# Kernel tuning notes

Hardware: AMD Instinct MI355X
Metric: run time of the kernel (lower is better)

Reference implementation:

```python
import jax, jax.numpy as jnp
import numpy as np
import math

B, S, H, HKV, DH = 2, 2048, 32, 1, 128  # batch, seq, q heads, kv heads, per-head/model dim
D_K = 128


def setup_inputs() -> dict:
    key = jax.random.key(0)
    ks = jax.random.split(key, 11)
    sc = 0.02
    return {
        "query": jax.random.normal(ks[0], (B, S, DH), jnp.float32),
        "key": jax.random.normal(ks[1], (B, S, DH), jnp.float32),
        "values": jax.random.normal(ks[2], (B, S, DH), jnp.float32),
        "W_q": jax.random.normal(ks[3], (DH, H * DH), jnp.float32) * sc,
        "b_q": jnp.zeros((H * DH,), jnp.float32),
        "W_k": jax.random.normal(ks[4], (DH, HKV * DH), jnp.float32) * sc,
        "b_k": jnp.zeros((HKV * DH,), jnp.float32),
        "W_v": jax.random.normal(ks[5], (DH, HKV * DH), jnp.float32) * sc,
        "b_v": jnp.zeros((HKV * DH,), jnp.float32),
        "W_o": jax.random.normal(ks[6], (H * DH, DH), jnp.float32) * sc,
        "b_o": jnp.zeros((DH,), jnp.float32),
    }


def reference(query, key, values, W_q, b_q, W_k, b_k, W_v, b_v, W_o, b_o):
    # Projections (note: the original uses raw .view(-1, H, S, DH), which we
    # replicate exactly — it is a reshape, not a transpose).
    q = (query @ W_q + b_q).reshape(-1, H, S, DH)      # [B,H,S,DH]
    k = (key @ W_k + b_k).reshape(-1, HKV, S, DH)       # [B,1,S,DH]
    v = (values @ W_v + b_v).reshape(-1, HKV, S, DH)    # [B,1,S,DH]

    # RoPE outputs in the original forward are computed but never used
    # (dead code), and mask defaults to None -> no masking. Dropout omitted
    # for deterministic reference.
    scores = jnp.matmul(q, jnp.swapaxes(k, -1, -2)) / math.sqrt(D_K)  # [B,H,S,S]
    attn = jax.nn.softmax(scores, axis=-1)
    out = jnp.matmul(attn, v)                           # [B,H,S,DH]
    out = jnp.swapaxes(out, 1, 2).reshape(-1, S, H * DH)
    return out @ W_o + b_o                              # [B,S,DH]
```

## Files before the change

kernel.cpp:

```cpp
#include <hip/hip_runtime.h>
#include <hip/hip_bf16.h>
#include <math.h>


typedef __hip_bfloat16 bf16;
typedef __attribute__((ext_vector_type(8))) short short8;
typedef __attribute__((ext_vector_type(4))) float floatx4;

static constexpr int B_ = 2;
static constexpr int S_ = 2048;
static constexpr int H_ = 32;
static constexpr int DH_ = 128;

#define GL16(gp, lp)                                              \
  __builtin_amdgcn_global_load_lds(                               \
      (const __attribute__((address_space(1))) void*)(gp),        \
      (__attribute__((address_space(3))) void*)(lp), 16, 0, 0)

static __device__ __forceinline__ unsigned bpack(float lo, float hi) {
  unsigned a = __float_as_uint(lo) + 0x8000u;
  unsigned b = __float_as_uint(hi) + 0x8000u;
  return __builtin_amdgcn_perm(b, a, 0x07060302u);
}

static __device__ __forceinline__ bool detect_f32(
    const unsigned short* __restrict__ q) {
  int t = threadIdx.x & 63;
  int cnt = 0;
#pragma unroll
  for (int i = 0; i < 8; ++i) {
    unsigned short u = q[t * 8 + i];
    int e = (u >> 7) & 0xFF;
    if (e < 0x60) cnt++;
  }
#pragma unroll
  for (int off = 1; off < 64; off <<= 1) cnt += __shfl_xor(cnt, off);
  return cnt >= 8;
}

static __device__ __forceinline__ short8 loadA8(const void* __restrict__ base,
                                                size_t elt, bool f) {
  if (f) {
    const float4* p = (const float4*)((const float*)base + elt);
    float4 x = p[0], y = p[1];
    union { unsigned u[4]; short8 v; } r;
    r.u[0] = bpack(x.x, x.y);
    r.u[1] = bpack(x.z, x.w);
    r.u[2] = bpack(y.x, y.y);
    r.u[3] = bpack(y.z, y.w);
    return r.v;
  }
  return *(const short8*)((const bf16*)base + elt);
}

static __device__ void do_ttranspose(const void* __restrict__ W,
                                     bf16* __restrict__ Wt, int K, int N,
                                     bool f, float scale, int bx, int by,
                                     bf16 (*tile)[66]) {
  int n0 = bx * 64, k0 = by * 64;
  int c = threadIdx.x & 63;
  int r4 = threadIdx.x >> 6;
#pragma unroll
  for (int i = 0; i < 16; ++i) {
    int r = r4 * 16 + i;
    float v = f ? ((const float*)W)[(size_t)(k0 + r) * N + n0 + c]
                : __bfloat162float(((const bf16*)W)[(size_t)(k0 + r) * N + n0 + c]);
    tile[r][c] = __float2bfloat16(v * scale);
  }
  __syncthreads();
#pragma unroll
  for (int i = 0; i < 16; ++i) {
    int cc = r4 * 16 + i;
    Wt[(size_t)(n0 + cc) * K + k0 + c] = tile[c][cc];
  }
}

__global__ void prep(const void* __restrict__ query,
                     const void* __restrict__ bq, const void* __restrict__ bk,
                     const void* __restrict__ bv, const void* __restrict__ bo,
                     float* __restrict__ fbq, float* __restrict__ fbk,
                     float* __restrict__ fbv, float* __restrict__ fbo,
                     const void* __restrict__ Wq, bf16* __restrict__ Wqt,
                     const void* __restrict__ Wk, bf16* __restrict__ Wkt,
                     const void* __restrict__ Wv, bf16* __restrict__ Wvt,
                     const void* __restrict__ Wo, bf16* __restrict__ Wot,
                     float qscale) {
  __shared__ bf16 tile[64][66];
  const int id = blockIdx.x;
  const bool f = detect_f32((const unsigned short*)query);
  if (id < 18) {
    int i = id * 256 + threadIdx.x;
    const void* s; float* d; int off; float sc = 1.f;
    if (i < 4096) { s = bq; d = fbq; off = i; sc = qscale; }
    else if (i < 4224) { s = bk; d = fbk; off = i - 4096; }
    else if (i < 4352) { s = bv; d = fbv; off = i - 4224; }
    else if (i < 4480) { s = bo; d = fbo; off = i - 4352; }
    else return;
    float v = f ? ((const float*)s)[off]
                : __bfloat162float(((const bf16*)s)[off]);
    d[off] = v * sc;
  } else if (id < 146) {
    int j = id - 18;
    do_ttranspose(Wq, Wqt, DH_, H_ * DH_, f, qscale, j % 64, j / 64, tile);
  } else if (id < 150) {
    int j = id - 146;
    do_ttranspose(Wk, Wkt, DH_, DH_, f, 1.0f, j % 2, j / 2, tile);
  } else if (id < 154) {
    int j = id - 150;
    do_ttranspose(Wv, Wvt, DH_, DH_, f, 1.0f, j % 2, j / 2, tile);
  } else {
    int j = id - 154;
    do_ttranspose(Wo, Wot, H_ * DH_, DH_, f, 1.0f, j % 2, j / 2, tile);
  }
}

__global__ __launch_bounds__(256) void gemm_qkv(
    const void* __restrict__ query, const void* __restrict__ key,
    const void* __restrict__ values, const bf16* __restrict__ Wqt,
    const bf16* __restrict__ Wkt, const bf16* __restrict__ Wvt,
    const float* __restrict__ fbq, const float* __restrict__ fbk,
    const float* __restrict__ fbv, bf16* __restrict__ Qp,
    bf16* __restrict__ Kp, bf16* __restrict__ Vtp) {
  const int bx = blockIdx.x;
  const void* A; const bf16* Bt; const float* bias; bf16* Cb;
  int mode, ldc, colb;
  if (bx < 64)      { A = query;  Bt = Wqt; bias = fbq; Cb = Qp;  mode = 0; ldc = 4096; colb = bx; }
  else if (bx < 66) { A = key;    Bt = Wkt; bias = fbk; Cb = Kp;  mode = 0; ldc = 128;  colb = bx - 64; }
  else              { A = values; Bt = Wvt; bias = fbv; Cb = Vtp; mode = 3; ldc = 0;    colb = bx - 66; }

  const bool f = detect_f32((const unsigned short*)query);
  const int lane = threadIdx.x & 63;
  const int wave = threadIdx.x >> 6;
  const int lm = lane & 15;
  const int quad = lane >> 4;
  const int row_base = blockIdx.y * 64 + wave * 16;
  const int col_base = colb * 64;

  const size_t aelt = (size_t)(row_base + lm) * DH_ + quad * 8;
  const bf16* brow = Bt + (size_t)(col_base + lm) * DH_ + quad * 8;

  floatx4 z = {0.f, 0.f, 0.f, 0.f};
  floatx4 acc[4] = {z, z, z, z};
#pragma unroll
  for (int kk = 0; kk < DH_; kk += 32) {
    short8 a = loadA8(A, aelt + kk, f);
#pragma unroll
    for (int t = 0; t < 4; ++t) {
      short8 b = *(const short8*)(brow + (size_t)(t * 16) * DH_ + kk);
      acc[t] = __builtin_amdgcn_mfma_f32_16x16x32_bf16(a, b, acc[t], 0, 0, 0);
    }
  }
#pragma unroll
  for (int t = 0; t < 4; ++t) {
    int col = col_base + t * 16 + lm;
#pragma unroll
    for (int r = 0; r < 4; ++r) {
      int row = row_base + quad * 4 + r;
      if (mode == 0) {
        Cb[(size_t)row * ldc + col] = __float2bfloat16(acc[t][r] + bias[col]);
      } else {
        Cb[((size_t)((row >> 11) * DH_ + col)) * S_ + (row & 2047)] =
            __float2bfloat16(acc[t][r] + bias[col]);
      }
    }
  }
}

__global__ __launch_bounds__(256) void gemm_out(
    const bf16* __restrict__ A, const bf16* __restrict__ Bt,
    float* __restrict__ Cf) {
  constexpr int K_len = (H_ * DH_) / 8;
  const int lane = threadIdx.x & 63;
  const int wave = threadIdx.x >> 6;
  const int lm = lane & 15;
  const int quad = lane >> 4;
  const int row_base = blockIdx.x * 64 + wave * 16;
  const int koff = blockIdx.y * K_len;

  const bf16* arow = A + (size_t)(row_base + lm) * (H_ * DH_) + koff + quad * 8;
  const bf16* brow = Bt + (size_t)lm * (H_ * DH_) + koff + quad * 8;

  floatx4 z = {0.f, 0.f, 0.f, 0.f};
  floatx4 acc[8] = {z, z, z, z, z, z, z, z};
#pragma unroll 2
  for (int kk = 0; kk < K_len; kk += 32) {
    short8 a = *(const short8*)(arow + kk);
#pragma unroll
    for (int t = 0; t < 8; ++t) {
      short8 b = *(const short8*)(brow + (size_t)(t * 16) * (H_ * DH_) + kk);
      acc[t] = __builtin_amdgcn_mfma_f32_16x16x32_bf16(a, b, acc[t], 0, 0, 0);
    }
  }
#pragma unroll
  for (int t = 0; t < 8; ++t) {
    int col = t * 16 + lm;
#pragma unroll
    for (int r = 0; r < 4; ++r) {
      int row = row_base + quad * 4 + r;
      Cf[(size_t)blockIdx.y * (4096 * 128) + (size_t)row * DH_ + col] =
          acc[t][r];
    }
  }
}

__global__ void finish_out(const float* __restrict__ parts,
                           const float* __restrict__ bias,
                           float* __restrict__ out) {
  int i = blockIdx.x * 256 + threadIdx.x;
  const float4* p = (const float4*)parts;
  float4 bb = ((const float4*)bias)[i & 31];
  float4 o = bb;
#pragma unroll
  for (int j = 0; j < 8; ++j) {
    float4 a = p[i + (size_t)j * 131072];
    o.x += a.x; o.y += a.y; o.z += a.z; o.w += a.w;
  }
  ((float4*)out)[i] = o;
}

static __device__ __forceinline__ float fexp2(float x) {
#if __has_builtin(__builtin_amdgcn_exp2f)
  return __builtin_amdgcn_exp2f(x);
#else
  return exp2f(x);
#endif
}

static __device__ __forceinline__ void pexchange(const unsigned pk[8],
                                                 int quad, short8* pf) {
  const bool q0 = (quad & 1);
  unsigned sA0 = q0 ? pk[0] : pk[2];
  unsigned sA1 = q0 ? pk[1] : pk[3];
  unsigned sA2 = q0 ? pk[4] : pk[6];
  unsigned sA3 = q0 ? pk[5] : pk[7];
  unsigned r0 = (unsigned)__shfl_xor((int)sA0, 16);
  unsigned r1 = (unsigned)__shfl_xor((int)sA1, 16);
  unsigned r2 = (unsigned)__shfl_xor((int)sA2, 16);
  unsigned r3 = (unsigned)__shfl_xor((int)sA3, 16);
  unsigned M0 = q0 ? r0 : pk[0];
  unsigned M1 = q0 ? r1 : pk[1];
  unsigned M2 = q0 ? pk[2] : r0;
  unsigned M3 = q0 ? pk[3] : r1;
  unsigned M4 = q0 ? r2 : pk[4];
  unsigned M5 = q0 ? r3 : pk[5];
  unsigned M6 = q0 ? pk[6] : r2;
  unsigned M7 = q0 ? pk[7] : r3;
  const bool swp = (quad == 1) || (quad == 2);
  union { unsigned u[4]; short8 v; } f0, f1;
  unsigned t0, t1;
  t0 = (unsigned)__shfl_xor((int)M0, 48); f0.u[0] = swp ? t0 : M0;
  t1 = (unsigned)__shfl_xor((int)M1, 48); f0.u[1] = swp ? t1 : M1;
  t0 = (unsigned)__shfl_xor((int)M2, 48); f0.u[2] = swp ? t0 : M2;
  t1 = (unsigned)__shfl_xor((int)M3, 48); f0.u[3] = swp ? t1 : M3;
  t0 = (unsigned)__shfl_xor((int)M4, 48); f1.u[0] = swp ? t0 : M4;
  t1 = (unsigned)__shfl_xor((int)M5, 48); f1.u[1] = swp ? t1 : M5;
  t0 = (unsigned)__shfl_xor((int)M6, 48); f1.u[2] = swp ? t0 : M6;
  t1 = (unsigned)__shfl_xor((int)M7, 48); f1.u[3] = swp ? t1 : M7;
  pf[0] = f0.v;
  pf[1] = f1.v;
}

__global__ __launch_bounds__(256, 2) void flash_attn(
    const bf16* __restrict__ Qp, const bf16* __restrict__ Kp,
    const bf16* __restrict__ Vt, bf16* __restrict__ O2c) {
  const int tid = threadIdx.x;
  const int lane = tid & 63;
  const int wave = tid >> 6;
  const int lm = lane & 15;
  const int quad = lane >> 4;
  const int qt = blockIdx.x;
  const int h = blockIdx.y;
  const int b = blockIdx.z;

  __shared__ __align__(16) bf16 Klds[64 * 128];
  __shared__ __align__(16) bf16 Vlds[2][128 * 64];

  const int base = qt * 128 + wave * 32;
  const bf16* qrow = Qp + ((size_t)b * S_ + h * 64 + (base >> 5)) * 4096;
  short8 qf0[4], qf1[4];
#pragma unroll
  for (int ks = 0; ks < 4; ++ks) {
    qf0[ks] = *(const short8*)(qrow + lm * 128 + quad * 8 + ks * 32);
    qf1[ks] = *(const short8*)(qrow + (16 + lm) * 128 + quad * 8 + ks * 32);
  }

  const bf16* Kb = Kp + (size_t)b * S_ * DH_;
  const bf16* Vb = Vt + (size_t)b * DH_ * S_;
  const int sw = lm & 7;

  const bf16* kgp[4];
  const bf16* vgp[4];
#pragma unroll
  for (int i = 0; i < 4; ++i) {
    const int inst = wave * 4 + i;
    const int krow = inst * 4 + quad;
    kgp[i] = Kb + (size_t)krow * 128 + ((lm ^ (krow & 7)) * 8);
    const int vrow = inst * 8 + (lane >> 3);
    vgp[i] = Vb + (size_t)vrow * S_ + (((lane & 7) ^ (vrow & 7)) * 8);
  }

  floatx4 z = {0.f, 0.f, 0.f, 0.f};
  floatx4 oa0[8], oa1[8];
#pragma unroll
  for (int nt = 0; nt < 8; ++nt) { oa0[nt] = z; oa1[nt] = z; }
  float ls0 = 0.f, ls1 = 0.f;

#pragma unroll
  for (int i = 0; i < 4; ++i) {
    GL16(kgp[i], &Klds[(wave * 4 + i) * 512]);
    GL16(vgp[i], &Vlds[0][(wave * 4 + i) * 512]);
    kgp[i] += 64 * 128;
    vgp[i] += 64;
  }

  int cur = 0;
  for (int kb = 0; kb < S_; kb += 64) {
    __syncthreads();
    const bool more = kb + 64 < S_;
    if (more) {
#pragma unroll
      for (int i = 0; i < 4; ++i) {
        GL16(vgp[i], &Vlds[cur ^ 1][(wave * 4 + i) * 512]);
        vgp[i] += 64;
      }
    }

    floatx4 s0[4] = {z, z, z, z}, s1[4] = {z, z, z, z};
    __builtin_amdgcn_s_setprio(1);
#pragma unroll
    for (int t = 0; t < 4; ++t) {
#pragma unroll
      for (int ks = 0; ks < 4; ++ks) {
        short8 kf = *(const short8*)(&Klds[(t * 16 + lm) * 128 +
                                           (((quad + 4 * ks) ^ sw) * 8)]);
        s0[t] = __builtin_amdgcn_mfma_f32_16x16x32_bf16(kf, qf0[ks], s0[t],
                                                        0, 0, 0);
        s1[t] = __builtin_amdgcn_mfma_f32_16x16x32_bf16(kf, qf1[ks], s1[t],
                                                        0, 0, 0);
      }
    }
    __builtin_amdgcn_s_setprio(0);

    __syncthreads();
    if (more) {
#pragma unroll
      for (int i = 0; i < 4; ++i) {
        GL16(kgp[i], &Klds[(wave * 4 + i) * 512]);
        kgp[i] += 64 * 128;
      }
    }

    unsigned pk0[8], pk1[8];
#pragma unroll
    for (int t = 0; t < 4; ++t) {
      float a0 = fexp2(s0[t][0]), a1 = fexp2(s0[t][1]);
      float a2 = fexp2(s0[t][2]), a3 = fexp2(s0[t][3]);
      ls0 += (a0 + a1) + (a2 + a3);
      pk0[2 * t] = bpack(a0, a1);
      pk0[2 * t + 1] = bpack(a2, a3);
      float c0 = fexp2(s1[t][0]), c1 = fexp2(s1[t][1]);
      float c2 = fexp2(s1[t][2]), c3 = fexp2(s1[t][3]);
      ls1 += (c0 + c1) + (c2 + c3);
      pk1[2 * t] = bpack(c0, c1);
      pk1[2 * t + 1] = bpack(c2, c3);
    }
    short8 pf0[2], pf1[2];
    pexchange(pk0, quad, pf0);
    pexchange(pk1, quad, pf1);

    __builtin_amdgcn_s_setprio(1);
#pragma unroll
    for (int ks2 = 0; ks2 < 2; ++ks2) {
#pragma unroll
      for (int nt = 0; nt < 8; ++nt) {
        short8 vf = *(const short8*)(&Vlds[cur][(nt * 16 + lm) * 64 +
                                              (((quad + 4 * ks2) ^ sw) * 8)]);
        oa0[nt] = __builtin_amdgcn_mfma_f32_16x16x32_bf16(pf0[ks2], vf,
                                                          oa0[nt], 0, 0, 0);
        oa1[nt] = __builtin_amdgcn_mfma_f32_16x16x32_bf16(pf1[ks2], vf,
                                                          oa1[nt], 0, 0, 0);
      }
    }
    __builtin_amdgcn_s_setprio(0);
    cur ^= 1;
  }

  ls0 += __shfl_xor(ls0, 16);
  ls0 += __shfl_xor(ls0, 32);
  ls1 += __shfl_xor(ls1, 16);
  ls1 += __shfl_xor(ls1, 32);
  float inv0[4], inv1[4];
#pragma unroll
  for (int r = 0; r < 4; ++r) {
    inv0[r] = 1.0f / __shfl(ls0, quad * 4 + r);
    inv1[r] = 1.0f / __shfl(ls1, quad * 4 + r);
  }

#pragma unroll
  for (int r = 0; r < 4; ++r) {
    int s2a = base + quad * 4 + r;
    int s2b = s2a + 16;
    size_t ba = ((size_t)b * S_ + s2a) * 4096 + (size_t)h * 128;
    size_t bb = ((size_t)b * S_ + s2b) * 4096 + (size_t)h * 128;
#pragma unroll
    for (int nt = 0; nt < 8; ++nt) {
      O2c[ba + nt * 16 + lm] = __float2bfloat16(oa0[nt][r] * inv0[r]);
      O2c[bb + nt * 16 + lm] = __float2bfloat16(oa1[nt][r] * inv1[r]);
    }
  }
}

extern "C" void kernel_launch(void* const* d_in, const int* in_sizes, int n_in,
                              void* d_out, int out_size, void* d_ws,
                              size_t ws_size, hipStream_t stream) {
  (void)in_sizes;
  (void)n_in;
  (void)out_size;
  (void)ws_size;

  const void* query = d_in[0];
  const void* key = d_in[1];
  const void* values = d_in[2];
  const void* W_q = d_in[3];
  const void* b_q = d_in[4];
  const void* W_k = d_in[5];
  const void* b_k = d_in[6];
  const void* W_v = d_in[7];
  const void* b_v = d_in[8];
  const void* W_o = d_in[9];
  const void* b_o = d_in[10];
  float* out = (float*)d_out;

  const float kScale = 0.1275174388204085f;
  const int M = B_ * S_;
  const int QN = B_ * S_ * DH_;

  char* w = (char*)d_ws;
  auto carve = [&](size_t bytes) -> char* {
    char* p = w;
    w += (bytes + 255) & ~(size_t)255;
    return p;
  };
  float* fbq = (float*)carve((size_t)H_ * DH_ * 4);
  float* fbk = (float*)carve((size_t)DH_ * 4);
  float* fbv = (float*)carve((size_t)DH_ * 4);
  float* fbo = (float*)carve((size_t)DH_ * 4);
  bf16* Wqt = (bf16*)carve((size_t)DH_ * H_ * DH_ * 2);
  bf16* Wkt = (bf16*)carve((size_t)DH_ * DH_ * 2);
  bf16* Wvt = (bf16*)carve((size_t)DH_ * DH_ * 2);
  bf16* Wot = (bf16*)carve((size_t)H_ * DH_ * DH_ * 2);
  bf16* Kp = (bf16*)carve((size_t)B_ * S_ * DH_ * 2);
  bf16* Vtp = (bf16*)carve((size_t)B_ * S_ * DH_ * 2);
  bf16* Qp = (bf16*)carve((size_t)M * H_ * DH_ * 2);
  bf16* O2c = (bf16*)carve((size_t)M * H_ * DH_ * 2);

  float* parts = (float*)Qp;

  prep<<<282, 256, 0, stream>>>(query, b_q, b_k, b_v, b_o, fbq, fbk, fbv,
                                fbo, W_q, Wqt, W_k, Wkt, W_v, Wvt, W_o, Wot,
                                kScale);

  gemm_qkv<<<dim3(68, 64), 256, 0, stream>>>(query, key, values, Wqt, Wkt,
                                             Wvt, fbq, fbk, fbv, Qp, Kp, Vtp);

  flash_attn<<<dim3(S_ / 128, H_, B_), 256, 0, stream>>>(Qp, Kp, Vtp, O2c);

  gemm_out<<<dim3(M / 64, 8), 256, 0, stream>>>(O2c, Wot, parts);

  finish_out<<<QN / 4 / 256, 256, 0, stream>>>(parts, fbo, out);
}
```

Measured before the change: 324.8 us.

## Fuse weight prep into QKV GEMM and widen output split-K

Removes the separate prep kernel: each QKV GEMM block converts and transposes its weight tile into shared memory and reuses it across eight row tiles, while extra blocks transpose W_o. Biases are read and converted directly where they are used. The output GEMM split-K is doubled to 16, so finish_out now sums 16 partials. This saves a launch and global weight round-trips, but adds more partial-sum memory traffic in the reduction.

```diff
diff --git a/kernel.cpp b/kernel.cpp
--- a/kernel.cpp
+++ b/kernel.cpp
@@ -75,92 +75,87 @@
   }
 }
 
-__global__ void prep(const void* __restrict__ query,
-                     const void* __restrict__ bq, const void* __restrict__ bk,
-                     const void* __restrict__ bv, const void* __restrict__ bo,
-                     float* __restrict__ fbq, float* __restrict__ fbk,
-                     float* __restrict__ fbv, float* __restrict__ fbo,
-                     const void* __restrict__ Wq, bf16* __restrict__ Wqt,
-                     const void* __restrict__ Wk, bf16* __restrict__ Wkt,
-                     const void* __restrict__ Wv, bf16* __restrict__ Wvt,
-                     const void* __restrict__ Wo, bf16* __restrict__ Wot,
-                     float qscale) {
-  __shared__ bf16 tile[64][66];
-  const int id = blockIdx.x;
-  const bool f = detect_f32((const unsigned short*)query);
-  if (id < 18) {
-    int i = id * 256 + threadIdx.x;
-    const void* s; float* d; int off; float sc = 1.f;
-    if (i < 4096) { s = bq; d = fbq; off = i; sc = qscale; }
-    else if (i < 4224) { s = bk; d = fbk; off = i - 4096; }
-    else if (i < 4352) { s = bv; d = fbv; off = i - 4224; }
-    else if (i < 4480) { s = bo; d = fbo; off = i - 4352; }
-    else return;
-    float v = f ? ((const float*)s)[off]
-                : __bfloat162float(((const bf16*)s)[off]);
-    d[off] = v * sc;
-  } else if (id < 146) {
-    int j = id - 18;
-    do_ttranspose(Wq, Wqt, DH_, H_ * DH_, f, qscale, j % 64, j / 64, tile);
-  } else if (id < 150) {
-    int j = id - 146;
-    do_ttranspose(Wk, Wkt, DH_, DH_, f, 1.0f, j % 2, j / 2, tile);
-  } else if (id < 154) {
-    int j = id - 150;
-    do_ttranspose(Wv, Wvt, DH_, DH_, f, 1.0f, j % 2, j / 2, tile);
-  } else {
-    int j = id - 154;
-    do_ttranspose(Wo, Wot, H_ * DH_, DH_, f, 1.0f, j % 2, j / 2, tile);
-  }
-}
-
 __global__ __launch_bounds__(256) void gemm_qkv(
     const void* __restrict__ query, const void* __restrict__ key,
-    const void* __restrict__ values, const bf16* __restrict__ Wqt,
-    const bf16* __restrict__ Wkt, const bf16* __restrict__ Wvt,
-    const float* __restrict__ fbq, const float* __restrict__ fbk,
-    const float* __restrict__ fbv, bf16* __restrict__ Qp,
-    bf16* __restrict__ Kp, bf16* __restrict__ Vtp) {
+    const void* __restrict__ values, const void* __restrict__ Wq,
+    const void* __restrict__ Wk, const void* __restrict__ Wv,
+    const void* __restrict__ Wo, const void* __restrict__ bq,
+    const void* __restrict__ bk, const void* __restrict__ bv,
+    bf16* __restrict__ Qp, bf16* __restrict__ Kp, bf16* __restrict__ Vtp,
+    bf16* __restrict__ Wot, float qscale) {
+  __shared__ __align__(16) bf16 sh[64 * 136];
+  const bool f = detect_f32((const unsigned short*)query);
   const int bx = blockIdx.x;
-  const void* A; const bf16* Bt; const float* bias; bf16* Cb;
-  int mode, ldc, colb;
-  if (bx < 64)      { A = query;  Bt = Wqt; bias = fbq; Cb = Qp;  mode = 0; ldc = 4096; colb = bx; }
-  else if (bx < 66) { A = key;    Bt = Wkt; bias = fbk; Cb = Kp;  mode = 0; ldc = 128;  colb = bx - 64; }
-  else              { A = values; Bt = Wvt; bias = fbv; Cb = Vtp; mode = 3; ldc = 0;    colb = bx - 66; }
-
-  const bool f = detect_f32((const unsigned short*)query);
+  const int yb = blockIdx.y;
+
+  if (bx >= 68) {
+    int j = (bx - 68) * 8 + yb;
+    do_ttranspose(Wo, Wot, H_ * DH_, DH_, f, 1.0f, j % 2, j / 2,
+                  (bf16(*)[66])sh);
+    return;
+  }
+
+  const void* A; const void* W; const void* bias; bf16* Cb;
+  int mode, ldc, colb, N; float wsc, bsc;
+  if (bx < 64)      { A = query;  W = Wq; bias = bq; Cb = Qp;  mode = 0; ldc = 4096; colb = bx;      N = 4096; wsc = qscale; bsc = qscale; }
+  else if (bx < 66) { A = key;    W = Wk; bias = bk; Cb = Kp;  mode = 0; ldc = 128;  colb = bx - 64; N = 128;  wsc = 1.f;    bsc = 1.f; }
+  else              { A = values; W = Wv; bias = bv; Cb = Vtp; mode = 3; ldc = 0;    colb = bx - 66; N = 128;  wsc = 1.f;    bsc = 1.f; }
+  const int col_base = colb * 64;
+
+  {
+    int c = threadIdx.x & 63, r4 = threadIdx.x >> 6;
+#pragma unroll
+    for (int i = 0; i < 32; ++i) {
+      int k = r4 * 32 + i;
+      float v = f ? ((const float*)W)[(size_t)k * N + col_base + c]
+                  : __bfloat162float(
+                        ((const bf16*)W)[(size_t)k * N + col_base + c]);
+      sh[c * 136 + k] = __float2bfloat16(v * wsc);
+    }
+  }
+
   const int lane = threadIdx.x & 63;
   const int wave = threadIdx.x >> 6;
   const int lm = lane & 15;
   const int quad = lane >> 4;
-  const int row_base = blockIdx.y * 64 + wave * 16;
-  const int col_base = colb * 64;
-
-  const size_t aelt = (size_t)(row_base + lm) * DH_ + quad * 8;
-  const bf16* brow = Bt + (size_t)(col_base + lm) * DH_ + quad * 8;
-
-  floatx4 z = {0.f, 0.f, 0.f, 0.f};
-  floatx4 acc[4] = {z, z, z, z};
-#pragma unroll
-  for (int kk = 0; kk < DH_; kk += 32) {
-    short8 a = loadA8(A, aelt + kk, f);
-#pragma unroll
-    for (int t = 0; t < 4; ++t) {
-      short8 b = *(const short8*)(brow + (size_t)(t * 16) * DH_ + kk);
-      acc[t] = __builtin_amdgcn_mfma_f32_16x16x32_bf16(a, b, acc[t], 0, 0, 0);
-    }
-  }
+
+  float bt[4];
 #pragma unroll
   for (int t = 0; t < 4; ++t) {
     int col = col_base + t * 16 + lm;
-#pragma unroll
-    for (int r = 0; r < 4; ++r) {
-      int row = row_base + quad * 4 + r;
-      if (mode == 0) {
-        Cb[(size_t)row * ldc + col] = __float2bfloat16(acc[t][r] + bias[col]);
-      } else {
-        Cb[((size_t)((row >> 11) * DH_ + col)) * S_ + (row & 2047)] =
-            __float2bfloat16(acc[t][r] + bias[col]);
+    float v = f ? ((const float*)bias)[col]
+                : __bfloat162float(((const bf16*)bias)[col]);
+    bt[t] = v * bsc;
+  }
+  __syncthreads();
+
+  floatx4 z = {0.f, 0.f, 0.f, 0.f};
+#pragma unroll
+  for (int rt = 0; rt < 8; ++rt) {
+    const int row_base = (yb * 8 + rt) * 64 + wave * 16;
+    const size_t aelt = (size_t)(row_base + lm) * DH_ + quad * 8;
+    floatx4 acc[4] = {z, z, z, z};
+#pragma unroll
+    for (int kk = 0; kk < DH_; kk += 32) {
+      short8 a = loadA8(A, aelt + kk, f);
+#pragma unroll
+      for (int t = 0; t < 4; ++t) {
+        short8 b = *(const short8*)(&sh[(t * 16 + lm) * 136 + quad * 8 + kk]);
+        acc[t] = __builtin_amdgcn_mfma_f32_16x16x32_bf16(a, b, acc[t], 0, 0, 0);
+      }
+    }
+#pragma unroll
+    for (int t = 0; t < 4; ++t) {
+      int col = col_base + t * 16 + lm;
+#pragma unroll
+      for (int r = 0; r < 4; ++r) {
+        int row = row_base + quad * 4 + r;
+        if (mode == 0) {
+          Cb[(size_t)row * ldc + col] = __float2bfloat16(acc[t][r] + bt[t]);
+        } else {
+          Cb[((size_t)((row >> 11) * DH_ + col)) * S_ + (row & 2047)] =
+              __float2bfloat16(acc[t][r] + bt[t]);
+        }
       }
     }
   }
@@ -169,7 +164,7 @@
 __global__ __launch_bounds__(256) void gemm_out(
     const bf16* __restrict__ A, const bf16* __restrict__ Bt,
     float* __restrict__ Cf) {
-  constexpr int K_len = (H_ * DH_) / 8;
+  constexpr int K_len = (H_ * DH_) / 16;
   const int lane = threadIdx.x & 63;
   const int wave = threadIdx.x >> 6;
   const int lm = lane & 15;
@@ -204,14 +199,25 @@
 }
 
 __global__ void finish_out(const float* __restrict__ parts,
-                           const float* __restrict__ bias,
+                           const void* __restrict__ bo_raw,
+                           const unsigned short* __restrict__ qdet,
                            float* __restrict__ out) {
+  const bool f = detect_f32(qdet);
   int i = blockIdx.x * 256 + threadIdx.x;
   const float4* p = (const float4*)parts;
-  float4 bb = ((const float4*)bias)[i & 31];
-  float4 o = bb;
-#pragma unroll
-  for (int j = 0; j < 8; ++j) {
+  float4 o;
+  int cb = (i & 31) * 4;
+  if (f) {
+    o = ((const float4*)bo_raw)[i & 31];
+  } else {
+    const bf16* bb = (const bf16*)bo_raw;
+    o.x = __bfloat162float(bb[cb + 0]);
+    o.y = __bfloat162float(bb[cb + 1]);
+    o.z = __bfloat162float(bb[cb + 2]);
+    o.w = __bfloat162float(bb[cb + 3]);
+  }
+#pragma unroll
+  for (int j = 0; j < 16; ++j) {
     float4 a = p[i + (size_t)j * 131072];
     o.x += a.x; o.y += a.y; o.z += a.z; o.w += a.w;
   }
@@ -441,13 +447,6 @@
     w += (bytes + 255) & ~(size_t)255;
     return p;
   };
-  float* fbq = (float*)carve((size_t)H_ * DH_ * 4);
-  float* fbk = (float*)carve((size_t)DH_ * 4);
-  float* fbv = (float*)carve((size_t)DH_ * 4);
-  float* fbo = (float*)carve((size_t)DH_ * 4);
-  bf16* Wqt = (bf16*)carve((size_t)DH_ * H_ * DH_ * 2);
-  bf16* Wkt = (bf16*)carve((size_t)DH_ * DH_ * 2);
-  bf16* Wvt = (bf16*)carve((size_t)DH_ * DH_ * 2);
   bf16* Wot = (bf16*)carve((size_t)H_ * DH_ * DH_ * 2);
   bf16* Kp = (bf16*)carve((size_t)B_ * S_ * DH_ * 2);
   bf16* Vtp = (bf16*)carve((size_t)B_ * S_ * DH_ * 2);
@@ -456,16 +455,14 @@
 
   float* parts = (float*)Qp;
 
-  prep<<<282, 256, 0, stream>>>(query, b_q, b_k, b_v, b_o, fbq, fbk, fbv,
-                                fbo, W_q, Wqt, W_k, Wkt, W_v, Wvt, W_o, Wot,
-                                kScale);
-
-  gemm_qkv<<<dim3(68, 64), 256, 0, stream>>>(query, key, values, Wqt, Wkt,
-                                             Wvt, fbq, fbk, fbv, Qp, Kp, Vtp);
+  gemm_qkv<<<dim3(84, 8), 256, 0, stream>>>(query, key, values, W_q, W_k,
+                                            W_v, W_o, b_q, b_k, b_v, Qp, Kp,
+                                            Vtp, Wot, kScale);
 
   flash_attn<<<dim3(S_ / 128, H_, B_), 256, 0, stream>>>(Qp, Kp, Vtp, O2c);
 
-  gemm_out<<<dim3(M / 64, 8), 256, 0, stream>>>(O2c, Wot, parts);
-
-  finish_out<<<QN / 4 / 256, 256, 0, stream>>>(parts, fbo, out);
-}
+  gemm_out<<<dim3(M / 64, 16), 256, 0, stream>>>(O2c, Wot, parts);
+
+  finish_out<<<QN / 4 / 256, 256, 0, stream>>>(
+      parts, b_o, (const unsigned short*)query, out);
+}
```

New measurement: 310.2 us, median of 2. 4.5% less time.
